# Optimization experiments

Measured on AMD Instinct MI355X. Metric: run time of the kernel, lower is better.

The kernel has to match this reference:

```python
import jax, jax.numpy as jnp
import numpy as np

S = 7
STEP = 1.0 / S
LAMBDA_COORD = 5.0
LAMBDA_NOOBJ = 0.5


def setup_inputs() -> dict:
    key = jax.random.key(0)
    k1, k2, k3 = jax.random.split(key, 3)
    B = 16384
    pred = jax.random.uniform(k1, (B, S, S, 30), dtype=jnp.float32)
    target = jax.random.uniform(k2, (B, S, S, 30), dtype=jnp.float32)
    conf = (jax.random.uniform(k3, (B, S, S)) > 0.9).astype(jnp.float32)
    target = target.at[..., 4].set(conf)
    return {"pred": pred, "target": target}


def _convert_box(box):
    # box: [..., S, S, 4] in cell-relative (x, y, w, h); returns clipped corners.
    gi = jnp.arange(S, dtype=box.dtype).reshape(1, S, 1)  # first spatial axis -> x offset
    gj = jnp.arange(S, dtype=box.dtype).reshape(1, 1, S)  # second spatial axis -> y offset
    x, y, w, h = box[..., 0], box[..., 1], box[..., 2], box[..., 3]
    cx = (x + gi) * STEP
    cy = (y + gj) * STEP
    x1 = jnp.maximum(cx - w / 2, 0.0)
    y1 = jnp.maximum(cy - h / 2, 0.0)
    x2 = jnp.minimum(cx + w / 2, 1.0)
    y2 = jnp.minimum(cy + h / 2, 1.0)
    return x1, y1, x2, y2


def _iou(b1, b2):
    a, b, c, d = b1
    q, w, e, r = b2
    minx = jnp.maximum(a, q)
    miny = jnp.maximum(b, w)
    maxx = jnp.minimum(c, e)
    maxy = jnp.minimum(d, r)
    inter = (maxy - miny) * (maxx - minx)  # faithful: no clamping of negative overlaps
    union = (e - q) * (r - w) + (d - b) * (c - a) - inter
    return jnp.where(inter > 0, inter / (union + 1e-05), 0.0)


def reference(pred, target):
    B = pred.shape[0]
    tbox = _convert_box(target[..., :4])
    pbox1 = _convert_box(pred[..., 0:4])
    pbox2 = _convert_box(pred[..., 5:9])
    iou1 = _iou(tbox, pbox1)  # [B, S, S]
    iou2 = _iou(tbox, pbox2)

    sel2 = iou1 <= iou2  # original: box1 responsible only if iou1 > iou2
    conf_t = jax.lax.stop_gradient(jnp.where(sel2, iou2, iou1))  # .item() detached iou
    pxy = jnp.where(sel2[..., None], pred[..., 5:7], pred[..., 0:2])
    pwh = jnp.where(sel2[..., None], pred[..., 7:9], pred[..., 2:4])
    pconf = jnp.where(sel2, pred[..., 9], pred[..., 4])

    obj = (target[..., 4] > 0).astype(pred.dtype)  # [B, S, S]
    noobj = (target[..., 4] == 0).astype(pred.dtype)

    obj_loss = jnp.sum(obj * (pconf - conf_t) ** 2)
    xy_loss = jnp.sum(obj[..., None] * (pxy - target[..., 0:2]) ** 2)
    wh_loss = jnp.sum(obj[..., None] * (pwh - target[..., 2:4]) ** 2)
    class_loss = jnp.sum(obj[..., None] * (pred[..., 10:] - target[..., 10:]) ** 2)
    noobj_loss = jnp.sum(noobj * ((pred[..., 4] - target[..., 4]) ** 2 + (pred[..., 9] - target[..., 9]) ** 2))

    loss = obj_loss + LAMBDA_NOOBJ * noobj_loss + LAMBDA_COORD * (xy_loss + wh_loss) + class_loss
    return loss / B
```

## Files before the change

kernel.cpp:

```cpp
#include <hip/hip_runtime.h>


#define NS 7
#define NC 30

__global__ void zero_out_kernel(float* out) { out[0] = 0.0f; }

__global__ __launch_bounds__(256) void yolo_loss_kernel(
    const float* __restrict__ pred,
    const float* __restrict__ targ,
    float* __restrict__ out,
    int n_cells, float inv_B)
{
    const float STEP = 1.0f / 7.0f;
    const float L_COORD = 5.0f;
    const float L_NOOBJ = 0.5f;

    int cell = blockIdx.x * blockDim.x + threadIdx.x;
    float lsum = 0.0f;
    if (cell < n_cells) {
        int j = cell % NS;
        int i = (cell / NS) % NS;
        float gi = (float)i;
        float gj = (float)j;

        const float2* p2 = (const float2*)pred + (size_t)cell * 15;
        const float2* t2 = (const float2*)targ + (size_t)cell * 15;
        float p[NC], t[NC];
        #pragma unroll
        for (int k = 0; k < 15; ++k) {
            float2 v = p2[k]; p[2 * k] = v.x; p[2 * k + 1] = v.y;
        }
        #pragma unroll
        for (int k = 0; k < 15; ++k) {
            float2 u = t2[k]; t[2 * k] = u.x; t[2 * k + 1] = u.y;
        }

        float ta, tb, tc, td;
        {
            float cx = (t[0] + gi) * STEP;
            float cy = (t[1] + gj) * STEP;
            ta = fmaxf(cx - t[2] * 0.5f, 0.0f);
            tb = fmaxf(cy - t[3] * 0.5f, 0.0f);
            tc = fminf(cx + t[2] * 0.5f, 1.0f);
            td = fminf(cy + t[3] * 0.5f, 1.0f);
        }
        float q1, w1, e1, r1;
        {
            float cx = (p[0] + gi) * STEP;
            float cy = (p[1] + gj) * STEP;
            q1 = fmaxf(cx - p[2] * 0.5f, 0.0f);
            w1 = fmaxf(cy - p[3] * 0.5f, 0.0f);
            e1 = fminf(cx + p[2] * 0.5f, 1.0f);
            r1 = fminf(cy + p[3] * 0.5f, 1.0f);
        }
        float q2, w2, e2, r2;
        {
            float cx = (p[5] + gi) * STEP;
            float cy = (p[6] + gj) * STEP;
            q2 = fmaxf(cx - p[7] * 0.5f, 0.0f);
            w2 = fmaxf(cy - p[8] * 0.5f, 0.0f);
            e2 = fminf(cx + p[7] * 0.5f, 1.0f);
            r2 = fminf(cy + p[8] * 0.5f, 1.0f);
        }

        float tarea = (td - tb) * (tc - ta);
        float iou1, iou2;
        {
            float minx = fmaxf(ta, q1), miny = fmaxf(tb, w1);
            float maxx = fminf(tc, e1), maxy = fminf(td, r1);
            float inter = (maxy - miny) * (maxx - minx);
            float uni = (e1 - q1) * (r1 - w1) + tarea - inter;
            iou1 = (inter > 0.0f) ? inter / (uni + 1e-5f) : 0.0f;
        }
        {
            float minx = fmaxf(ta, q2), miny = fmaxf(tb, w2);
            float maxx = fminf(tc, e2), maxy = fminf(td, r2);
            float inter = (maxy - miny) * (maxx - minx);
            float uni = (e2 - q2) * (r2 - w2) + tarea - inter;
            iou2 = (inter > 0.0f) ? inter / (uni + 1e-5f) : 0.0f;
        }

        bool sel2 = (iou1 <= iou2);
        float conf_t = sel2 ? iou2 : iou1;
        float px = sel2 ? p[5] : p[0];
        float py = sel2 ? p[6] : p[1];
        float pw = sel2 ? p[7] : p[2];
        float ph = sel2 ? p[8] : p[3];
        float pconf = sel2 ? p[9] : p[4];

        float obj = (t[4] > 0.0f) ? 1.0f : 0.0f;
        float noobj = (t[4] == 0.0f) ? 1.0f : 0.0f;

        float dx = px - t[0], dy = py - t[1];
        float dw = pw - t[2], dh = ph - t[3];
        float coord = dx * dx + dy * dy + dw * dw + dh * dh;

        float dc = pconf - conf_t;
        float obj_loss = dc * dc;

        float cls = 0.0f;
        #pragma unroll
        for (int k = 10; k < NC; ++k) {
            float d = p[k] - t[k];
            cls += d * d;
        }

        float d4 = p[4] - t[4];
        float d9 = p[9] - t[9];
        float noobj_loss = d4 * d4 + d9 * d9;

        lsum = obj * (obj_loss + L_COORD * coord + cls) + L_NOOBJ * noobj * noobj_loss;
    }

    #pragma unroll
    for (int off = 32; off > 0; off >>= 1)
        lsum += __shfl_down(lsum, off, 64);

    __shared__ float wsum[4];
    int lane = threadIdx.x & 63;
    int wid = threadIdx.x >> 6;
    if (lane == 0) wsum[wid] = lsum;
    __syncthreads();
    if (threadIdx.x == 0) {
        float s = (wsum[0] + wsum[1]) + (wsum[2] + wsum[3]);
        atomicAdd(out, s * inv_B);
    }
}

extern "C" void kernel_launch(void* const* d_in, const int* in_sizes, int n_in,
                              void* d_out, int out_size, void* d_ws, size_t ws_size,
                              hipStream_t stream) {
    const float* pred = (const float*)d_in[0];
    const float* targ = (const float*)d_in[1];
    float* out = (float*)d_out;

    const int B = 16384;
    const int n_cells = B * NS * NS;
    const float inv_B = 1.0f / (float)B;

    zero_out_kernel<<<1, 1, 0, stream>>>(out);

    const int block = 256;
    const int grid = (n_cells + block - 1) / block;
    yolo_loss_kernel<<<grid, block, 0, stream>>>(pred, targ, out, n_cells, inv_B);
}
```

Baseline: 204.1 us.

## Stage cell data through shared memory with coalesced float4 loads

Each block first copies its 256 cells of pred and target into shared memory with contiguous float4 loads, then each thread reads its own 30-float record from LDS. The earlier kernel had each thread read 120-byte strided records straight from global memory, giving poorly coalesced accesses. The change uses about 60 KB of LDS per block, which limits occupancy and adds a barrier. It also drops the bounds check because the cell count divides evenly, and replaces the zeroing kernel with a memset.

```diff
diff --git a/kernel.cpp b/kernel.cpp
--- a/kernel.cpp
+++ b/kernel.cpp
@@ -3,126 +3,140 @@
 
 #define NS 7
 #define NC 30
-
-__global__ void zero_out_kernel(float* out) { out[0] = 0.0f; }
+#define CPB 256
+#define F4_PER_CHUNK (CPB * NC / 4)
 
 __global__ __launch_bounds__(256) void yolo_loss_kernel(
     const float* __restrict__ pred,
     const float* __restrict__ targ,
-    float* __restrict__ out,
-    int n_cells, float inv_B)
+    float* __restrict__ out, float inv_B)
 {
     const float STEP = 1.0f / 7.0f;
     const float L_COORD = 5.0f;
     const float L_NOOBJ = 0.5f;
 
-    int cell = blockIdx.x * blockDim.x + threadIdx.x;
-    float lsum = 0.0f;
-    if (cell < n_cells) {
-        int j = cell % NS;
-        int i = (cell / NS) % NS;
-        float gi = (float)i;
-        float gj = (float)j;
+    __shared__ float sp[CPB * NC];
+    __shared__ float st[CPB * NC];
 
-        const float2* p2 = (const float2*)pred + (size_t)cell * 15;
-        const float2* t2 = (const float2*)targ + (size_t)cell * 15;
-        float p[NC], t[NC];
+    const int tid = threadIdx.x;
+    const size_t base_f = (size_t)blockIdx.x * (CPB * NC);
+
+    {
+        const float4* __restrict__ gp4 = (const float4*)(pred + base_f);
+        const float4* __restrict__ gt4 = (const float4*)(targ + base_f);
+        float4* sp4 = (float4*)sp;
+        float4* st4 = (float4*)st;
         #pragma unroll
-        for (int k = 0; k < 15; ++k) {
-            float2 v = p2[k]; p[2 * k] = v.x; p[2 * k + 1] = v.y;
+        for (int k = tid; k < F4_PER_CHUNK; k += 256) {
+            sp4[k] = gp4[k];
+            st4[k] = gt4[k];
         }
+    }
+    __syncthreads();
+
+    const int cell = blockIdx.x * CPB + tid;
+    const int j = cell % NS;
+    const int i = (cell / NS) % NS;
+    const float gi = (float)i;
+    const float gj = (float)j;
+
+    float p[NC], t[NC];
+    {
+        const float2* lp2 = (const float2*)(sp + tid * NC);
+        const float2* lt2 = (const float2*)(st + tid * NC);
         #pragma unroll
-        for (int k = 0; k < 15; ++k) {
-            float2 u = t2[k]; t[2 * k] = u.x; t[2 * k + 1] = u.y;
+        for (int k = 0; k < NC / 2; ++k) {
+            float2 v = lp2[k]; p[2 * k] = v.x; p[2 * k + 1] = v.y;
+            float2 u = lt2[k]; t[2 * k] = u.x; t[2 * k + 1] = u.y;
         }
+    }
 
-        float ta, tb, tc, td;
-        {
-            float cx = (t[0] + gi) * STEP;
-            float cy = (t[1] + gj) * STEP;
-            ta = fmaxf(cx - t[2] * 0.5f, 0.0f);
-            tb = fmaxf(cy - t[3] * 0.5f, 0.0f);
-            tc = fminf(cx + t[2] * 0.5f, 1.0f);
-            td = fminf(cy + t[3] * 0.5f, 1.0f);
-        }
-        float q1, w1, e1, r1;
-        {
-            float cx = (p[0] + gi) * STEP;
-            float cy = (p[1] + gj) * STEP;
-            q1 = fmaxf(cx - p[2] * 0.5f, 0.0f);
-            w1 = fmaxf(cy - p[3] * 0.5f, 0.0f);
-            e1 = fminf(cx + p[2] * 0.5f, 1.0f);
-            r1 = fminf(cy + p[3] * 0.5f, 1.0f);
-        }
-        float q2, w2, e2, r2;
-        {
-            float cx = (p[5] + gi) * STEP;
-            float cy = (p[6] + gj) * STEP;
-            q2 = fmaxf(cx - p[7] * 0.5f, 0.0f);
-            w2 = fmaxf(cy - p[8] * 0.5f, 0.0f);
-            e2 = fminf(cx + p[7] * 0.5f, 1.0f);
-            r2 = fminf(cy + p[8] * 0.5f, 1.0f);
-        }
+    float ta, tb, tc, td;
+    {
+        float cx = (t[0] + gi) * STEP;
+        float cy = (t[1] + gj) * STEP;
+        ta = fmaxf(cx - t[2] * 0.5f, 0.0f);
+        tb = fmaxf(cy - t[3] * 0.5f, 0.0f);
+        tc = fminf(cx + t[2] * 0.5f, 1.0f);
+        td = fminf(cy + t[3] * 0.5f, 1.0f);
+    }
+    float q1, w1, e1, r1;
+    {
+        float cx = (p[0] + gi) * STEP;
+        float cy = (p[1] + gj) * STEP;
+        q1 = fmaxf(cx - p[2] * 0.5f, 0.0f);
+        w1 = fmaxf(cy - p[3] * 0.5f, 0.0f);
+        e1 = fminf(cx + p[2] * 0.5f, 1.0f);
+        r1 = fminf(cy + p[3] * 0.5f, 1.0f);
+    }
+    float q2, w2, e2, r2;
+    {
+        float cx = (p[5] + gi) * STEP;
+        float cy = (p[6] + gj) * STEP;
+        q2 = fmaxf(cx - p[7] * 0.5f, 0.0f);
+        w2 = fmaxf(cy - p[8] * 0.5f, 0.0f);
+        e2 = fminf(cx + p[7] * 0.5f, 1.0f);
+        r2 = fminf(cy + p[8] * 0.5f, 1.0f);
+    }
 
-        float tarea = (td - tb) * (tc - ta);
-        float iou1, iou2;
-        {
-            float minx = fmaxf(ta, q1), miny = fmaxf(tb, w1);
-            float maxx = fminf(tc, e1), maxy = fminf(td, r1);
-            float inter = (maxy - miny) * (maxx - minx);
-            float uni = (e1 - q1) * (r1 - w1) + tarea - inter;
-            iou1 = (inter > 0.0f) ? inter / (uni + 1e-5f) : 0.0f;
-        }
-        {
-            float minx = fmaxf(ta, q2), miny = fmaxf(tb, w2);
-            float maxx = fminf(tc, e2), maxy = fminf(td, r2);
-            float inter = (maxy - miny) * (maxx - minx);
-            float uni = (e2 - q2) * (r2 - w2) + tarea - inter;
-            iou2 = (inter > 0.0f) ? inter / (uni + 1e-5f) : 0.0f;
-        }
+    float tarea = (td - tb) * (tc - ta);
+    float iou1, iou2;
+    {
+        float minx = fmaxf(ta, q1), miny = fmaxf(tb, w1);
+        float maxx = fminf(tc, e1), maxy = fminf(td, r1);
+        float inter = (maxy - miny) * (maxx - minx);
+        float uni = (e1 - q1) * (r1 - w1) + tarea - inter;
+        iou1 = (inter > 0.0f) ? inter / (uni + 1e-5f) : 0.0f;
+    }
+    {
+        float minx = fmaxf(ta, q2), miny = fmaxf(tb, w2);
+        float maxx = fminf(tc, e2), maxy = fminf(td, r2);
+        float inter = (maxy - miny) * (maxx - minx);
+        float uni = (e2 - q2) * (r2 - w2) + tarea - inter;
+        iou2 = (inter > 0.0f) ? inter / (uni + 1e-5f) : 0.0f;
+    }
 
-        bool sel2 = (iou1 <= iou2);
-        float conf_t = sel2 ? iou2 : iou1;
-        float px = sel2 ? p[5] : p[0];
-        float py = sel2 ? p[6] : p[1];
-        float pw = sel2 ? p[7] : p[2];
-        float ph = sel2 ? p[8] : p[3];
-        float pconf = sel2 ? p[9] : p[4];
+    bool sel2 = (iou1 <= iou2);
+    float conf_t = sel2 ? iou2 : iou1;
+    float px = sel2 ? p[5] : p[0];
+    float py = sel2 ? p[6] : p[1];
+    float pw = sel2 ? p[7] : p[2];
+    float ph = sel2 ? p[8] : p[3];
+    float pconf = sel2 ? p[9] : p[4];
 
-        float obj = (t[4] > 0.0f) ? 1.0f : 0.0f;
-        float noobj = (t[4] == 0.0f) ? 1.0f : 0.0f;
+    float obj = (t[4] > 0.0f) ? 1.0f : 0.0f;
+    float noobj = (t[4] == 0.0f) ? 1.0f : 0.0f;
 
-        float dx = px - t[0], dy = py - t[1];
-        float dw = pw - t[2], dh = ph - t[3];
-        float coord = dx * dx + dy * dy + dw * dw + dh * dh;
+    float dx = px - t[0], dy = py - t[1];
+    float dw = pw - t[2], dh = ph - t[3];
+    float coord = dx * dx + dy * dy + dw * dw + dh * dh;
 
-        float dc = pconf - conf_t;
-        float obj_loss = dc * dc;
+    float dc = pconf - conf_t;
+    float obj_loss = dc * dc;
 
-        float cls = 0.0f;
-        #pragma unroll
-        for (int k = 10; k < NC; ++k) {
-            float d = p[k] - t[k];
-            cls += d * d;
-        }
+    float cls = 0.0f;
+    #pragma unroll
+    for (int k = 10; k < NC; ++k) {
+        float d = p[k] - t[k];
+        cls += d * d;
+    }
 
-        float d4 = p[4] - t[4];
-        float d9 = p[9] - t[9];
-        float noobj_loss = d4 * d4 + d9 * d9;
+    float d4 = p[4] - t[4];
+    float d9 = p[9] - t[9];
+    float noobj_loss = d4 * d4 + d9 * d9;
 
-        lsum = obj * (obj_loss + L_COORD * coord + cls) + L_NOOBJ * noobj * noobj_loss;
-    }
+    float lsum = obj * (obj_loss + L_COORD * coord + cls) + L_NOOBJ * noobj * noobj_loss;
 
     #pragma unroll
     for (int off = 32; off > 0; off >>= 1)
         lsum += __shfl_down(lsum, off, 64);
 
     __shared__ float wsum[4];
-    int lane = threadIdx.x & 63;
-    int wid = threadIdx.x >> 6;
+    int lane = tid & 63;
+    int wid = tid >> 6;
     if (lane == 0) wsum[wid] = lsum;
     __syncthreads();
-    if (threadIdx.x == 0) {
+    if (tid == 0) {
         float s = (wsum[0] + wsum[1]) + (wsum[2] + wsum[3]);
         atomicAdd(out, s * inv_B);
     }
@@ -139,9 +153,8 @@
     const int n_cells = B * NS * NS;
     const float inv_B = 1.0f / (float)B;
 
-    zero_out_kernel<<<1, 1, 0, stream>>>(out);
+    hipMemsetAsync(out, 0, sizeof(float) * out_size, stream);
 
-    const int block = 256;
-    const int grid = (n_cells + block - 1) / block;
-    yolo_loss_kernel<<<grid, block, 0, stream>>>(pred, targ, out, n_cells, inv_B);
+    const int grid = n_cells / CPB;
+    yolo_loss_kernel<<<grid, 256, 0, stream>>>(pred, targ, out, inv_B);
 }
```

New measurement: 209.4 us. 2.6% more time.
